# Optimization experiments

Hardware: AMD Instinct MI355X
Metric: run time of the kernel (lower is better)

## Reference

```python
import jax, jax.numpy as jnp
import numpy as np

N_ENTITIES = 100000
EMBED_DIM = 128
N_EDGES = 1600000
LEAKY_SLOPE = 0.01  # nn.LeakyReLU default


def setup_inputs() -> dict:
    key = jax.random.key(0)
    k1, k2, k3, k4, k5, k6, k7, k8 = jax.random.split(key, 8)
    entity_embs = jax.random.normal(k1, (N_ENTITIES, EMBED_DIM), dtype=jnp.float32)
    adj_rows = jax.random.randint(k2, (N_EDGES,), 0, N_ENTITIES, dtype=jnp.int32)
    adj_cols = jax.random.randint(k3, (N_EDGES,), 0, N_ENTITIES, dtype=jnp.int32)
    adj_vals = jax.random.uniform(k4, (N_EDGES,), dtype=jnp.float32)
    s = 1.0 / np.sqrt(EMBED_DIM)  # nn.Linear default init scale
    W_self = jax.random.uniform(k5, (EMBED_DIM, EMBED_DIM), jnp.float32, -s, s)
    b_self = jax.random.uniform(k6, (EMBED_DIM,), jnp.float32, -s, s)
    W_neigh = jax.random.uniform(k7, (EMBED_DIM, EMBED_DIM), jnp.float32, -s, s)
    b_neigh = jax.random.uniform(k8, (EMBED_DIM,), jnp.float32, -s, s)
    return {"entity_embs": entity_embs, "adj_rows": adj_rows, "adj_cols": adj_cols,
            "adj_vals": adj_vals, "W_self": W_self, "b_self": b_self,
            "W_neigh": W_neigh, "b_neigh": b_neigh}


def reference(entity_embs, adj_rows, adj_cols, adj_vals, W_self, b_self, W_neigh, b_neigh):
    # self path: Linear(input_dim, output_dim) -> x @ W.T + b
    self_emb = entity_embs @ W_self.T + b_self  # [N, D]
    # neighbor path: sparse adjacency SpMM (COO): out[r] += v * embs[c]
    contrib = adj_vals[:, None] * entity_embs[adj_cols]  # [E, D]
    neigh = jax.ops.segment_sum(contrib, adj_rows, num_segments=N_ENTITIES)  # [N, D]
    neigh_emb = neigh @ W_neigh.T + b_neigh
    out = jax.nn.leaky_relu(self_emb + neigh_emb, negative_slope=LEAKY_SLOPE)
    # dropout is identity in eval mode
    return out
```

## Files before the change

kernel.cpp:

```cpp
#include <hip/hip_runtime.h>

#define DIM 128
#define TILE_R 32
#define CAP 64
#define NREG 8
#define NCHUNK 256

typedef __attribute__((ext_vector_type(8))) short short8;
typedef __attribute__((ext_vector_type(4))) float floatx4;

static __device__ __forceinline__ short f2bf(float x) {
    unsigned u = __float_as_uint(x);
    u = (u + 0x7FFF + ((u >> 16) & 1)) >> 16;
    return (short)u;
}
static __device__ __forceinline__ float bflo(unsigned p) { return __uint_as_float(p << 16); }
static __device__ __forceinline__ float bfhi(unsigned p) { return __uint_as_float(p & 0xFFFF0000u); }

static __device__ __forceinline__ unsigned packcv(int c, float v) {
    int q = (int)(v * 32768.f + 0.5f);
    q = q > 32767 ? 32767 : q;
    return ((unsigned)c << 15) | (unsigned)q;
}

__global__ __launch_bounds__(256) void zero_kernel(float4* __restrict__ out, int n4) {
    int i = blockIdx.x * 256 + threadIdx.x;
    if (i < n4) out[i] = make_float4(0.f, 0.f, 0.f, 0.f);
}

__global__ __launch_bounds__(256) void zero_counts_kernel(int* __restrict__ cnt,
                                                          int* __restrict__ cursor, int n) {
    int i = blockIdx.x * 256 + threadIdx.x;
    if (i < n) cnt[i] = 0;
    if (i == 0) *cursor = 0;
}

__global__ __launch_bounds__(256) void prep_kernel(const float* __restrict__ Wself,
                                                   const float* __restrict__ Wneigh,
                                                   short* __restrict__ Wf,
                                                   int* __restrict__ next, int nRows) {
    int idx = blockIdx.x * 256 + threadIdx.x;
    if (idx < 4096) {
        int t = idx >> 8;
        int s = (idx >> 6) & 3;
        int lane = idx & 63;
        int n = (t & 7) * 16 + (lane & 15);
        int k0 = s * 32 + (lane >> 4) * 8;
        const float* row = (t < 8 ? Wself : Wneigh) + (size_t)n * DIM + k0;
        short8 v;
#pragma unroll
        for (int j = 0; j < 8; j++) v[j] = f2bf(row[j]);
        *(short8*)(Wf + (size_t)idx * 8) = v;
    }
    int r = idx - 4096;
    if (r >= 0 && r < nRows) next[r] = r * CAP;
}

__global__ __launch_bounds__(256) void pack_kernel(const int* __restrict__ cols,
                                                   const float* __restrict__ vals,
                                                   unsigned* __restrict__ pe, int nE) {
    int i4 = (blockIdx.x * 256 + threadIdx.x) * 4;
    if (i4 + 3 < nE) {
        int4 c = *(const int4*)(cols + i4);
        float4 v = *(const float4*)(vals + i4);
        uint4 o;
        o.x = packcv(c.x, v.x);
        o.y = packcv(c.y, v.y);
        o.z = packcv(c.z, v.z);
        o.w = packcv(c.w, v.w);
        *(uint4*)(pe + i4) = o;
    } else {
        for (int k = 0; k < 4 && i4 + k < nE; k++) pe[i4 + k] = packcv(cols[i4 + k], vals[i4 + k]);
    }
}

__global__ __launch_bounds__(256) void fill_xcd_pk_kernel(const int* __restrict__ rows,
                                                          const unsigned* __restrict__ pe,
                                                          int* __restrict__ next,
                                                          unsigned* __restrict__ pk,
                                                          int nE, int nRows) {
    int region = blockIdx.x & (NREG - 1);
    int chunk = blockIdx.x / NREG;
    int rowsPerReg = (nRows + NREG - 1) / NREG;
    int rowLo = region * rowsPerReg;
    int rowHi = min(rowLo + rowsPerReg, nRows);
    int per = (nE + NCHUNK - 1) / NCHUNK;
    per = (per + 7) & ~7;
    int s = chunk * per;
    int e = min(s + per, nE);

    for (int base = s + threadIdx.x * 8; base < e; base += 256 * 8) {
        int r8[8];
        unsigned p8[8];
        int cnt = 8;
        if (base + 7 < e) {
            int4 rv0 = *(const int4*)(rows + base);
            int4 rv1 = *(const int4*)(rows + base + 4);
            uint4 pv0 = *(const uint4*)(pe + base);
            uint4 pv1 = *(const uint4*)(pe + base + 4);
            r8[0] = rv0.x; r8[1] = rv0.y; r8[2] = rv0.z; r8[3] = rv0.w;
            r8[4] = rv1.x; r8[5] = rv1.y; r8[6] = rv1.z; r8[7] = rv1.w;
            p8[0] = pv0.x; p8[1] = pv0.y; p8[2] = pv0.z; p8[3] = pv0.w;
            p8[4] = pv1.x; p8[5] = pv1.y; p8[6] = pv1.z; p8[7] = pv1.w;
        } else {
            cnt = e - base;
            for (int k = 0; k < cnt; k++) {
                r8[k] = rows[base + k];
                p8[k] = pe[base + k];
            }
        }
#pragma unroll 8
        for (int k = 0; k < cnt; k++) {
            int rr = r8[k];
            if (rr >= rowLo && rr < rowHi) {
                int p = atomicAdd(&next[rr], 1);
                if (p < rr * CAP + CAP) pk[p] = p8[k];
            }
        }
    }
}

__global__ __launch_bounds__(256) void hist_kernel(const int* __restrict__ rows,
                                                   int* __restrict__ cnt, int nE) {
    int i4 = (blockIdx.x * 256 + threadIdx.x) * 4;
    if (i4 + 3 < nE) {
        int4 r = *(const int4*)(rows + i4);
        atomicAdd(&cnt[r.x], 1);
        atomicAdd(&cnt[r.y], 1);
        atomicAdd(&cnt[r.z], 1);
        atomicAdd(&cnt[r.w], 1);
    } else {
        for (int k = 0; k < 4 && i4 + k < nE; k++) atomicAdd(&cnt[rows[i4 + k]], 1);
    }
}

__global__ __launch_bounds__(256) void offsets_kernel(int* __restrict__ next,
                                                      int* __restrict__ start,
                                                      int* __restrict__ cursor, int n) {
    int i = blockIdx.x * 256 + threadIdx.x;
    int lane = threadIdx.x & 63;
    int c = (i < n) ? next[i] : 0;
    int s = c;
#pragma unroll
    for (int d = 1; d < 64; d <<= 1) {
        int t = __shfl_up(s, d);
        if (lane >= d) s += t;
    }
    int total = __shfl(s, 63);
    int base = 0;
    if (lane == 63) base = atomicAdd(cursor, total);
    base = __shfl(base, 63);
    int off = base + s - c;
    if (i < n) {
        start[i] = off;
        next[i] = off;
    }
}

__global__ __launch_bounds__(256) void fillB_kernel(const int* __restrict__ rows,
                                                    const int* __restrict__ cols,
                                                    const float* __restrict__ vals,
                                                    int* __restrict__ next,
                                                    int2* __restrict__ csr, int nE) {
    int i4 = (blockIdx.x * 256 + threadIdx.x) * 4;
    if (i4 + 3 < nE) {
        int4 r = *(const int4*)(rows + i4);
        int4 c = *(const int4*)(cols + i4);
        float4 v = *(const float4*)(vals + i4);
        int p0 = atomicAdd(&next[r.x], 1);
        int p1 = atomicAdd(&next[r.y], 1);
        int p2 = atomicAdd(&next[r.z], 1);
        int p3 = atomicAdd(&next[r.w], 1);
        csr[p0] = make_int2(c.x, __float_as_int(v.x));
        csr[p1] = make_int2(c.y, __float_as_int(v.y));
        csr[p2] = make_int2(c.z, __float_as_int(v.z));
        csr[p3] = make_int2(c.w, __float_as_int(v.w));
    } else {
        for (int k = 0; k < 4 && i4 + k < nE; k++) {
            int p = atomicAdd(&next[rows[i4 + k]], 1);
            csr[p] = make_int2(cols[i4 + k], __float_as_int(vals[i4 + k]));
        }
    }
}

__global__ __launch_bounds__(256) void wprep_kernel(const float* __restrict__ Wself,
                                                    const float* __restrict__ Wneigh,
                                                    short* __restrict__ Wf) {
    int idx = blockIdx.x * 256 + threadIdx.x;
    int t = idx >> 8;
    int s = (idx >> 6) & 3;
    int lane = idx & 63;
    int n = (t & 7) * 16 + (lane & 15);
    int k0 = s * 32 + (lane >> 4) * 8;
    const float* row = (t < 8 ? Wself : Wneigh) + (size_t)n * DIM + k0;
    short8 v;
#pragma unroll
    for (int j = 0; j < 8; j++) v[j] = f2bf(row[j]);
    *(short8*)(Wf + (size_t)idx * 8) = v;
}

__global__ __launch_bounds__(256) void gemm4_kernel(const float* __restrict__ embs,
                                                    const short* __restrict__ Wf,
                                                    unsigned short* __restrict__ Sb,
                                                    unsigned short* __restrict__ Yb,
                                                    int nRows) {
    int wave = threadIdx.x >> 6;
    int lane = threadIdx.x & 63;
    int quad = lane >> 4;
    int m0 = blockIdx.x * 256 + wave * 64;

    short8 a[4][4];
#pragma unroll
    for (int rt = 0; rt < 4; rt++) {
        int m = m0 + rt * 16 + (lane & 15);
        bool valid = m < nRows;
        const float* Arow = embs + (size_t)m * DIM;
#pragma unroll
        for (int s = 0; s < 4; s++) {
            float4 f0 = make_float4(0.f, 0.f, 0.f, 0.f), f1 = f0;
            if (valid) {
                f0 = *(const float4*)(Arow + s * 32 + quad * 8);
                f1 = *(const float4*)(Arow + s * 32 + quad * 8 + 4);
            }
            short8 av;
            av[0] = f2bf(f0.x); av[1] = f2bf(f0.y); av[2] = f2bf(f0.z); av[3] = f2bf(f0.w);
            av[4] = f2bf(f1.x); av[5] = f2bf(f1.y); av[6] = f2bf(f1.z); av[7] = f2bf(f1.w);
            a[rt][s] = av;
        }
    }

    const short8* WfV = (const short8*)Wf;
#pragma unroll
    for (int t = 0; t < 16; t++) {
        floatx4 acc0 = {0.f, 0.f, 0.f, 0.f};
        floatx4 acc1 = acc0, acc2 = acc0, acc3 = acc0;
#pragma unroll
        for (int s = 0; s < 4; s++) {
            short8 b = WfV[(t * 4 + s) * 64 + lane];
            acc0 = __builtin_amdgcn_mfma_f32_16x16x32_bf16(a[0][s], b, acc0, 0, 0, 0);
            acc1 = __builtin_amdgcn_mfma_f32_16x16x32_bf16(a[1][s], b, acc1, 0, 0, 0);
            acc2 = __builtin_amdgcn_mfma_f32_16x16x32_bf16(a[2][s], b, acc2, 0, 0, 0);
            acc3 = __builtin_amdgcn_mfma_f32_16x16x32_bf16(a[3][s], b, acc3, 0, 0, 0);
        }
        int col = t * 16 + (lane & 15);
        unsigned short* dst = (col < DIM) ? (Sb + col) : (Yb + (col - DIM));
#pragma unroll
        for (int reg = 0; reg < 4; reg++) {
            int g0 = m0 + quad * 4 + reg;
            int g1 = g0 + 16, g2 = g0 + 32, g3 = g0 + 48;
            if (g0 < nRows) dst[(size_t)g0 * DIM] = (unsigned short)f2bf(acc0[reg]);
            if (g1 < nRows) dst[(size_t)g1 * DIM] = (unsigned short)f2bf(acc1[reg]);
            if (g2 < nRows) dst[(size_t)g2 * DIM] = (unsigned short)f2bf(acc2[reg]);
            if (g3 < nRows) dst[(size_t)g3 * DIM] = (unsigned short)f2bf(acc3[reg]);
        }
    }
}

__global__ __launch_bounds__(256) void gatherY_pk_kernel(const unsigned* __restrict__ Sb,
                                                         const unsigned* __restrict__ Yb,
                                                         const int* __restrict__ rowEnd,
                                                         const unsigned* __restrict__ pk,
                                                         const float* __restrict__ bself,
                                                         const float* __restrict__ bneigh,
                                                         float* __restrict__ out, int nRows) {
    int r = blockIdx.x * 4 + (threadIdx.x >> 6);
    if (r >= nRows) return;
    int lane = threadIdx.x & 63;
    int s = r * CAP;
    int e = min(__builtin_amdgcn_readfirstlane(rowEnd[r]), s + CAP);
    float ax = 0.f, ay = 0.f;
    const float qs = 1.f / 32768.f;
    int j = s;
    for (; j + 4 <= e; j += 4) {
        uint4 q = *(const uint4*)(pk + j);
        unsigned y0 = Yb[(size_t)(q.x >> 15) * 64 + lane];
        unsigned y1 = Yb[(size_t)(q.y >> 15) * 64 + lane];
        unsigned y2 = Yb[(size_t)(q.z >> 15) * 64 + lane];
        unsigned y3 = Yb[(size_t)(q.w >> 15) * 64 + lane];
        float v0 = (float)(q.x & 32767u) * qs;
        float v1 = (float)(q.y & 32767u) * qs;
        float v2 = (float)(q.z & 32767u) * qs;
        float v3 = (float)(q.w & 32767u) * qs;
        ax += v0 * bflo(y0) + v1 * bflo(y1) + v2 * bflo(y2) + v3 * bflo(y3);
        ay += v0 * bfhi(y0) + v1 * bfhi(y1) + v2 * bfhi(y2) + v3 * bfhi(y3);
    }
    for (; j < e; j++) {
        unsigned q = pk[j];
        float v = (float)(q & 32767u) * qs;
        unsigned y = Yb[(size_t)(q >> 15) * 64 + lane];
        ax += v * bflo(y);
        ay += v * bfhi(y);
    }
    unsigned sp = __builtin_nontemporal_load(&Sb[(size_t)r * 64 + lane]);
    float ox = bflo(sp) + bself[2 * lane] + bneigh[2 * lane] + ax;
    float oy = bfhi(sp) + bself[2 * lane + 1] + bneigh[2 * lane + 1] + ay;
    ox = ox > 0.f ? ox : 0.01f * ox;
    oy = oy > 0.f ? oy : 0.01f * oy;
    union { float2 f; double d; } u;
    u.f = make_float2(ox, oy);
    __builtin_nontemporal_store(u.d, (double*)(out + (size_t)r * DIM + lane * 2));
}

__global__ __launch_bounds__(256) void gatherY_kernel(const unsigned* __restrict__ Sb,
                                                      const unsigned* __restrict__ Yb,
                                                      const int* __restrict__ start,
                                                      const int* __restrict__ next,
                                                      const int2* __restrict__ csr,
                                                      const float* __restrict__ bself,
                                                      const float* __restrict__ bneigh,
                                                      float* __restrict__ out, int nRows) {
    int r = blockIdx.x * 4 + (threadIdx.x >> 6);
    if (r >= nRows) return;
    int lane = threadIdx.x & 63;
    int s = __builtin_amdgcn_readfirstlane(start[r]);
    int e = __builtin_amdgcn_readfirstlane(next[r]);
    float ax = 0.f, ay = 0.f;
    int j = s;
    for (; j + 4 <= e; j += 4) {
        int2 c0 = csr[j], c1 = csr[j + 1], c2 = csr[j + 2], c3 = csr[j + 3];
        unsigned y0 = Yb[(size_t)c0.x * 64 + lane];
        unsigned y1 = Yb[(size_t)c1.x * 64 + lane];
        unsigned y2 = Yb[(size_t)c2.x * 64 + lane];
        unsigned y3 = Yb[(size_t)c3.x * 64 + lane];
        float v0 = __int_as_float(c0.y), v1 = __int_as_float(c1.y);
        float v2 = __int_as_float(c2.y), v3 = __int_as_float(c3.y);
        ax += v0 * bflo(y0) + v1 * bflo(y1) + v2 * bflo(y2) + v3 * bflo(y3);
        ay += v0 * bfhi(y0) + v1 * bfhi(y1) + v2 * bfhi(y2) + v3 * bfhi(y3);
    }
    for (; j < e; j++) {
        int2 c = csr[j];
        float v = __int_as_float(c.y);
        unsigned y = Yb[(size_t)c.x * 64 + lane];
        ax += v * bflo(y);
        ay += v * bfhi(y);
    }
    unsigned sp = __builtin_nontemporal_load(&Sb[(size_t)r * 64 + lane]);
    float ox = bflo(sp) + bself[2 * lane] + bneigh[2 * lane] + ax;
    float oy = bfhi(sp) + bself[2 * lane + 1] + bneigh[2 * lane + 1] + ay;
    ox = ox > 0.f ? ox : 0.01f * ox;
    oy = oy > 0.f ? oy : 0.01f * oy;
    union { float2 f; double d; } u;
    u.f = make_float2(ox, oy);
    __builtin_nontemporal_store(u.d, (double*)(out + (size_t)r * DIM + lane * 2));
}

__global__ __launch_bounds__(256) void gather_embs_kernel(const float2* __restrict__ embs2,
                                                          const int* __restrict__ start,
                                                          const int* __restrict__ next,
                                                          const int2* __restrict__ csr,
                                                          float* __restrict__ out, int nRows) {
    int r = blockIdx.x * 4 + (threadIdx.x >> 6);
    if (r >= nRows) return;
    int lane = threadIdx.x & 63;
    int s = start[r];
    int e = next[r];
    float2 acc = make_float2(0.f, 0.f);
    for (int b = s; b < e; b += 64) {
        int n = min(64, e - b);
        int2 cv = make_int2(0, 0);
        if (lane < n) cv = csr[b + lane];
        float vf = __int_as_float(cv.y);
        for (int j = 0; j < n; j++) {
            int cj = __shfl(cv.x, j);
            float vj = __shfl(vf, j);
            float2 x = embs2[(size_t)cj * 64 + lane];
            acc.x += vj * x.x;
            acc.y += vj * x.y;
        }
    }
    ((float2*)out)[(size_t)r * 64 + lane] = acc;
}

__global__ __launch_bounds__(256) void scatter_kernel(
    const float* __restrict__ embs, const int* __restrict__ rows,
    const int* __restrict__ cols, const float* __restrict__ vals,
    float* __restrict__ out, int nE) {
    int e = blockIdx.x * 4 + (threadIdx.x >> 6);
    if (e >= nE) return;
    int lane = threadIdx.x & 63;
    int r = rows[e];
    int c = cols[e];
    float v = vals[e];
    float2 x = ((const float2*)(embs + (size_t)c * DIM))[lane];
    float* dst = out + (size_t)r * DIM + lane * 2;
    unsafeAtomicAdd(dst, v * x.x);
    unsafeAtomicAdd(dst + 1, v * x.y);
}

__global__ __launch_bounds__(256) void fused_kernel(
    const float* __restrict__ embs, const float* __restrict__ Wself,
    const float* __restrict__ bself, const float* __restrict__ Wneigh,
    const float* __restrict__ bneigh, float* __restrict__ out, int nRows) {
    __shared__ float xs[TILE_R][DIM];
    __shared__ float xn[TILE_R][DIM];

    int r0 = blockIdx.x * TILE_R;
    if (r0 >= nRows) return;

    const float4* gs = (const float4*)(embs + (size_t)r0 * DIM);
    const float4* gn = (const float4*)(out + (size_t)r0 * DIM);
    float4* sxs = (float4*)&xs[0][0];
    float4* sxn = (float4*)&xn[0][0];
    for (int i = threadIdx.x; i < TILE_R * DIM / 4; i += 256) {
        sxs[i] = gs[i];
        sxn[i] = gn[i];
    }
    __syncthreads();

    int j = threadIdx.x & 127;
    int rbase = (threadIdx.x >> 7) * 16;

    const float4* ws = (const float4*)(Wself + (size_t)j * DIM);
    const float4* wn = (const float4*)(Wneigh + (size_t)j * DIM);

    float acc[16];
#pragma unroll
    for (int i = 0; i < 16; i++) acc[i] = 0.f;

    for (int k4 = 0; k4 < DIM / 4; k4++) {
        float4 a = ws[k4];
        float4 b = wn[k4];
#pragma unroll
        for (int rr = 0; rr < 16; rr++) {
            float4 x = *(const float4*)&xs[rbase + rr][k4 * 4];
            float4 y = *(const float4*)&xn[rbase + rr][k4 * 4];
            acc[rr] += x.x * a.x + x.y * a.y + x.z * a.z + x.w * a.w
                     + y.x * b.x + y.y * b.y + y.z * b.z + y.w * b.w;
        }
    }

    float bias = bself[j] + bneigh[j];
#pragma unroll
    for (int rr = 0; rr < 16; rr++) {
        float v = acc[rr] + bias;
        out[(size_t)(r0 + rbase + rr) * DIM + j] = v > 0.f ? v : 0.01f * v;
    }
}

static inline size_t a16(size_t x) { return (x + 15) & ~(size_t)15; }

extern "C" void kernel_launch(void* const* d_in, const int* in_sizes, int n_in,
                              void* d_out, int out_size, void* d_ws, size_t ws_size,
                              hipStream_t stream) {
    const float* embs   = (const float*)d_in[0];
    const int*   rows   = (const int*)d_in[1];
    const int*   cols   = (const int*)d_in[2];
    const float* vals   = (const float*)d_in[3];
    const float* Wself  = (const float*)d_in[4];
    const float* bself  = (const float*)d_in[5];
    const float* Wneigh = (const float*)d_in[6];
    const float* bneigh = (const float*)d_in[7];
    float* out = (float*)d_out;

    int nE = in_sizes[1];
    int nRows = out_size / DIM;
    size_t wfBytes = (size_t)16 * 4 * 64 * 8 * 2;
    size_t bfPlane = (size_t)nRows * DIM * 2;

    size_t A7_next = 0;
    size_t A7_buck = A7_next + a16((size_t)nRows * 4);
    size_t A7_pe   = A7_buck + a16((size_t)nRows * CAP * 4);
    size_t A7_wf   = A7_pe + a16((size_t)nE * 4);
    size_t A7_y    = A7_wf + a16(wfBytes);
    size_t A7_s    = A7_y + bfPlane;
    size_t needA7  = A7_s + bfPlane;
    bool   okA7    = nRows <= (1 << 17);

    size_t B_next  = 0;
    size_t B_start = B_next + a16((size_t)nRows * 4);
    size_t B_cur   = B_start + a16((size_t)nRows * 4);
    size_t B_csr   = B_cur + 16;
    size_t B_wf    = B_csr + a16((size_t)nE * 8);
    size_t B_y     = B_wf + a16(wfBytes);
    size_t B_s     = B_y + bfPlane;
    size_t needB   = B_s + bfPlane;

    size_t C_csr  = a16((size_t)(2 * nRows + 1) * 4);
    size_t needC  = C_csr + (size_t)nE * 8;

    int rb = (nRows + 255) / 256;
    int eb4 = (nE / 4 + 255) / 256;
    int ebp = ((nE + 3) / 4 + 255) / 256;

    if (okA7 && ws_size >= needA7) {
        int*      next = (int*)((char*)d_ws + A7_next);
        unsigned* pk   = (unsigned*)((char*)d_ws + A7_buck);
        unsigned* pe   = (unsigned*)((char*)d_ws + A7_pe);
        short*    Wf   = (short*)((char*)d_ws + A7_wf);
        unsigned short* Yb = (unsigned short*)((char*)d_ws + A7_y);
        unsigned short* Sb = (unsigned short*)((char*)d_ws + A7_s);

        prep_kernel<<<(4096 + nRows + 255) / 256, 256, 0, stream>>>(Wself, Wneigh, Wf, next, nRows);
        pack_kernel<<<ebp, 256, 0, stream>>>(cols, vals, pe, nE);
        fill_xcd_pk_kernel<<<NREG * NCHUNK, 256, 0, stream>>>(rows, pe, next, pk, nE, nRows);
        gemm4_kernel<<<(nRows + 255) / 256, 256, 0, stream>>>(embs, Wf, Sb, Yb, nRows);
        gatherY_pk_kernel<<<(nRows + 3) / 4, 256, 0, stream>>>(
            (const unsigned*)Sb, (const unsigned*)Yb, next, pk, bself, bneigh, out, nRows);
    } else if (ws_size >= needB) {
        int*  next   = (int*)((char*)d_ws + B_next);
        int*  start  = (int*)((char*)d_ws + B_start);
        int*  cursor = (int*)((char*)d_ws + B_cur);
        int2* csr    = (int2*)((char*)d_ws + B_csr);
        short* Wf    = (short*)((char*)d_ws + B_wf);
        unsigned short* Yb = (unsigned short*)((char*)d_ws + B_y);
        unsigned short* Sb = (unsigned short*)((char*)d_ws + B_s);

        zero_counts_kernel<<<rb, 256, 0, stream>>>(next, cursor, nRows);
        hist_kernel<<<eb4, 256, 0, stream>>>(rows, next, nE);
        offsets_kernel<<<rb, 256, 0, stream>>>(next, start, cursor, nRows);
        fillB_kernel<<<eb4, 256, 0, stream>>>(rows, cols, vals, next, csr, nE);
        wprep_kernel<<<16, 256, 0, stream>>>(Wself, Wneigh, Wf);
        gemm4_kernel<<<(nRows + 255) / 256, 256, 0, stream>>>(embs, Wf, Sb, Yb, nRows);
        gatherY_kernel<<<(nRows + 3) / 4, 256, 0, stream>>>(
            (const unsigned*)Sb, (const unsigned*)Yb, start, next, csr,
            bself, bneigh, out, nRows);
    } else if (ws_size >= needC) {
        int* next = (int*)d_ws;
        int* start = next + nRows;
        int* cursor = start + nRows;
        int2* csr = (int2*)((char*)d_ws + C_csr);

        zero_counts_kernel<<<rb, 256, 0, stream>>>(next, cursor, nRows);
        hist_kernel<<<eb4, 256, 0, stream>>>(rows, next, nE);
        offsets_kernel<<<rb, 256, 0, stream>>>(next, start, cursor, nRows);
        fillB_kernel<<<eb4, 256, 0, stream>>>(rows, cols, vals, next, csr, nE);
        gather_embs_kernel<<<(nRows + 3) / 4, 256, 0, stream>>>(
            (const float2*)embs, start, next, csr, out, nRows);
        fused_kernel<<<(nRows + TILE_R - 1) / TILE_R, 256, 0, stream>>>(
            embs, Wself, bself, Wneigh, bneigh, out, nRows);
    } else {
        int n4 = out_size / 4;
        zero_kernel<<<(n4 + 255) / 256, 256, 0, stream>>>((float4*)out, n4);
        scatter_kernel<<<(nE + 3) / 4, 256, 0, stream>>>(embs, rows, cols, vals, out, nE);
        fused_kernel<<<(nRows + TILE_R - 1) / TILE_R, 256, 0, stream>>>(
            embs, Wself, bself, Wneigh, bneigh, out, nRows);
    }
}
```

Measured before the change: 295.0 us.

## Merge pack/prep kernels and run fill alongside GEMM in one launch

Combines the weight-prep/next-init kernel with the edge packing kernel into one launch, and combines the bucket-fill atomics with the bf16 MFMA GEMM in a single kernel whose first blocks do the GEMM and the remaining blocks do the fill. This drops two launches and lets the compute-bound GEMM overlap with the atomic-bound fill. The cost is that the GEMM blocks occupy registers that may reduce fill occupancy, and the block ordering decides how much the two phases actually overlap.

```diff
diff --git a/kernel.cpp b/kernel.cpp
--- a/kernel.cpp
+++ b/kernel.cpp
@@ -35,10 +35,14 @@
     if (i == 0) *cursor = 0;
 }
 
-__global__ __launch_bounds__(256) void prep_kernel(const float* __restrict__ Wself,
-                                                   const float* __restrict__ Wneigh,
-                                                   short* __restrict__ Wf,
-                                                   int* __restrict__ next, int nRows) {
+__global__ __launch_bounds__(256) void packprep_kernel(const int* __restrict__ cols,
+                                                       const float* __restrict__ vals,
+                                                       unsigned* __restrict__ pe,
+                                                       const float* __restrict__ Wself,
+                                                       const float* __restrict__ Wneigh,
+                                                       short* __restrict__ Wf,
+                                                       int* __restrict__ next,
+                                                       int nE, int nRows) {
     int idx = blockIdx.x * 256 + threadIdx.x;
     if (idx < 4096) {
         int t = idx >> 8;
@@ -54,12 +58,8 @@
     }
     int r = idx - 4096;
     if (r >= 0 && r < nRows) next[r] = r * CAP;
-}
-
-__global__ __launch_bounds__(256) void pack_kernel(const int* __restrict__ cols,
-                                                   const float* __restrict__ vals,
-                                                   unsigned* __restrict__ pe, int nE) {
-    int i4 = (blockIdx.x * 256 + threadIdx.x) * 4;
+
+    int i4 = idx * 4;
     if (i4 + 3 < nE) {
         int4 c = *(const int4*)(cols + i4);
         float4 v = *(const float4*)(vals + i4);
@@ -74,47 +74,106 @@
     }
 }
 
-__global__ __launch_bounds__(256) void fill_xcd_pk_kernel(const int* __restrict__ rows,
-                                                          const unsigned* __restrict__ pe,
-                                                          int* __restrict__ next,
-                                                          unsigned* __restrict__ pk,
-                                                          int nE, int nRows) {
-    int region = blockIdx.x & (NREG - 1);
-    int chunk = blockIdx.x / NREG;
-    int rowsPerReg = (nRows + NREG - 1) / NREG;
-    int rowLo = region * rowsPerReg;
-    int rowHi = min(rowLo + rowsPerReg, nRows);
-    int per = (nE + NCHUNK - 1) / NCHUNK;
-    per = (per + 7) & ~7;
-    int s = chunk * per;
-    int e = min(s + per, nE);
-
-    for (int base = s + threadIdx.x * 8; base < e; base += 256 * 8) {
-        int r8[8];
-        unsigned p8[8];
-        int cnt = 8;
-        if (base + 7 < e) {
-            int4 rv0 = *(const int4*)(rows + base);
-            int4 rv1 = *(const int4*)(rows + base + 4);
-            uint4 pv0 = *(const uint4*)(pe + base);
-            uint4 pv1 = *(const uint4*)(pe + base + 4);
-            r8[0] = rv0.x; r8[1] = rv0.y; r8[2] = rv0.z; r8[3] = rv0.w;
-            r8[4] = rv1.x; r8[5] = rv1.y; r8[6] = rv1.z; r8[7] = rv1.w;
-            p8[0] = pv0.x; p8[1] = pv0.y; p8[2] = pv0.z; p8[3] = pv0.w;
-            p8[4] = pv1.x; p8[5] = pv1.y; p8[6] = pv1.z; p8[7] = pv1.w;
-        } else {
-            cnt = e - base;
+__global__ __launch_bounds__(256) void fillgemm_kernel(const int* __restrict__ rows,
+                                                       const unsigned* __restrict__ pe,
+                                                       int* __restrict__ next,
+                                                       unsigned* __restrict__ pk,
+                                                       int nE, int nRows,
+                                                       const float* __restrict__ embs,
+                                                       const short* __restrict__ Wf,
+                                                       unsigned short* __restrict__ Sb,
+                                                       unsigned short* __restrict__ Yb,
+                                                       int gemmBlocks) {
+    if ((int)blockIdx.x < gemmBlocks) {
+        int wave = threadIdx.x >> 6;
+        int lane = threadIdx.x & 63;
+        int quad = lane >> 4;
+        int m0 = blockIdx.x * 256 + wave * 64;
+
+        short8 a[4][4];
+#pragma unroll
+        for (int rt = 0; rt < 4; rt++) {
+            int m = m0 + rt * 16 + (lane & 15);
+            bool valid = m < nRows;
+            const float* Arow = embs + (size_t)m * DIM;
+#pragma unroll
+            for (int s = 0; s < 4; s++) {
+                float4 f0 = make_float4(0.f, 0.f, 0.f, 0.f), f1 = f0;
+                if (valid) {
+                    f0 = *(const float4*)(Arow + s * 32 + quad * 8);
+                    f1 = *(const float4*)(Arow + s * 32 + quad * 8 + 4);
+                }
+                short8 av;
+                av[0] = f2bf(f0.x); av[1] = f2bf(f0.y); av[2] = f2bf(f0.z); av[3] = f2bf(f0.w);
+                av[4] = f2bf(f1.x); av[5] = f2bf(f1.y); av[6] = f2bf(f1.z); av[7] = f2bf(f1.w);
+                a[rt][s] = av;
+            }
+        }
+
+        const short8* WfV = (const short8*)Wf;
+#pragma unroll
+        for (int t = 0; t < 16; t++) {
+            floatx4 acc0 = {0.f, 0.f, 0.f, 0.f};
+            floatx4 acc1 = acc0, acc2 = acc0, acc3 = acc0;
+#pragma unroll
+            for (int s = 0; s < 4; s++) {
+                short8 b = WfV[(t * 4 + s) * 64 + lane];
+                acc0 = __builtin_amdgcn_mfma_f32_16x16x32_bf16(a[0][s], b, acc0, 0, 0, 0);
+                acc1 = __builtin_amdgcn_mfma_f32_16x16x32_bf16(a[1][s], b, acc1, 0, 0, 0);
+                acc2 = __builtin_amdgcn_mfma_f32_16x16x32_bf16(a[2][s], b, acc2, 0, 0, 0);
+                acc3 = __builtin_amdgcn_mfma_f32_16x16x32_bf16(a[3][s], b, acc3, 0, 0, 0);
+            }
+            int col = t * 16 + (lane & 15);
+            unsigned short* dst = (col < DIM) ? (Sb + col) : (Yb + (col - DIM));
+#pragma unroll
+            for (int reg = 0; reg < 4; reg++) {
+                int g0 = m0 + quad * 4 + reg;
+                int g1 = g0 + 16, g2 = g0 + 32, g3 = g0 + 48;
+                if (g0 < nRows) dst[(size_t)g0 * DIM] = (unsigned short)f2bf(acc0[reg]);
+                if (g1 < nRows) dst[(size_t)g1 * DIM] = (unsigned short)f2bf(acc1[reg]);
+                if (g2 < nRows) dst[(size_t)g2 * DIM] = (unsigned short)f2bf(acc2[reg]);
+                if (g3 < nRows) dst[(size_t)g3 * DIM] = (unsigned short)f2bf(acc3[reg]);
+            }
+        }
+    } else {
+        int bid = blockIdx.x - gemmBlocks;
+        int region = bid & (NREG - 1);
+        int chunk = bid / NREG;
+        int rowsPerReg = (nRows + NREG - 1) / NREG;
+        int rowLo = region * rowsPerReg;
+        int rowHi = min(rowLo + rowsPerReg, nRows);
+        int per = (nE + NCHUNK - 1) / NCHUNK;
+        per = (per + 7) & ~7;
+        int s = chunk * per;
+        int e = min(s + per, nE);
+
+        for (int base = s + threadIdx.x * 8; base < e; base += 256 * 8) {
+            int r8[8];
+            unsigned p8[8];
+            int cnt = 8;
+            if (base + 7 < e) {
+                int4 rv0 = *(const int4*)(rows + base);
+                int4 rv1 = *(const int4*)(rows + base + 4);
+                uint4 pv0 = *(const uint4*)(pe + base);
+                uint4 pv1 = *(const uint4*)(pe + base + 4);
+                r8[0] = rv0.x; r8[1] = rv0.y; r8[2] = rv0.z; r8[3] = rv0.w;
+                r8[4] = rv1.x; r8[5] = rv1.y; r8[6] = rv1.z; r8[7] = rv1.w;
+                p8[0] = pv0.x; p8[1] = pv0.y; p8[2] = pv0.z; p8[3] = pv0.w;
+                p8[4] = pv1.x; p8[5] = pv1.y; p8[6] = pv1.z; p8[7] = pv1.w;
+            } else {
+                cnt = e - base;
+                for (int k = 0; k < cnt; k++) {
+                    r8[k] = rows[base + k];
+                    p8[k] = pe[base + k];
+                }
+            }
+#pragma unroll 8
             for (int k = 0; k < cnt; k++) {
-                r8[k] = rows[base + k];
-                p8[k] = pe[base + k];
-            }
-        }
-#pragma unroll 8
-        for (int k = 0; k < cnt; k++) {
-            int rr = r8[k];
-            if (rr >= rowLo && rr < rowHi) {
-                int p = atomicAdd(&next[rr], 1);
-                if (p < rr * CAP + CAP) pk[p] = p8[k];
+                int rr = r8[k];
+                if (rr >= rowLo && rr < rowHi) {
+                    int p = atomicAdd(&next[rr], 1);
+                    if (p < rr * CAP + CAP) pk[p] = p8[k];
+                }
             }
         }
     }
@@ -457,14 +516,14 @@
     size_t wfBytes = (size_t)16 * 4 * 64 * 8 * 2;
     size_t bfPlane = (size_t)nRows * DIM * 2;
 
-    size_t A7_next = 0;
-    size_t A7_buck = A7_next + a16((size_t)nRows * 4);
-    size_t A7_pe   = A7_buck + a16((size_t)nRows * CAP * 4);
-    size_t A7_wf   = A7_pe + a16((size_t)nE * 4);
-    size_t A7_y    = A7_wf + a16(wfBytes);
-    size_t A7_s    = A7_y + bfPlane;
-    size_t needA7  = A7_s + bfPlane;
-    bool   okA7    = nRows <= (1 << 17);
+    size_t A9_next = 0;
+    size_t A9_buck = A9_next + a16((size_t)nRows * 4);
+    size_t A9_pe   = A9_buck + a16((size_t)nRows * CAP * 4);
+    size_t A9_wf   = A9_pe + a16((size_t)nE * 4);
+    size_t A9_y    = A9_wf + a16(wfBytes);
+    size_t A9_s    = A9_y + bfPlane;
+    size_t needA9  = A9_s + bfPlane;
+    bool   okA9    = nRows <= (1 << 17);
 
     size_t B_next  = 0;
     size_t B_start = B_next + a16((size_t)nRows * 4);
@@ -482,18 +541,23 @@
     int eb4 = (nE / 4 + 255) / 256;
     int ebp = ((nE + 3) / 4 + 255) / 256;
 
-    if (okA7 && ws_size >= needA7) {
-        int*      next = (int*)((char*)d_ws + A7_next);
-        unsigned* pk   = (unsigned*)((char*)d_ws + A7_buck);
-        unsigned* pe   = (unsigned*)((char*)d_ws + A7_pe);
-        short*    Wf   = (short*)((char*)d_ws + A7_wf);
-        unsigned short* Yb = (unsigned short*)((char*)d_ws + A7_y);
-        unsigned short* Sb = (unsigned short*)((char*)d_ws + A7_s);
-
-        prep_kernel<<<(4096 + nRows + 255) / 256, 256, 0, stream>>>(Wself, Wneigh, Wf, next, nRows);
-        pack_kernel<<<ebp, 256, 0, stream>>>(cols, vals, pe, nE);
-        fill_xcd_pk_kernel<<<NREG * NCHUNK, 256, 0, stream>>>(rows, pe, next, pk, nE, nRows);
-        gemm4_kernel<<<(nRows + 255) / 256, 256, 0, stream>>>(embs, Wf, Sb, Yb, nRows);
+    if (okA9 && ws_size >= needA9) {
+        int*      next = (int*)((char*)d_ws + A9_next);
+        unsigned* pk   = (unsigned*)((char*)d_ws + A9_buck);
+        unsigned* pe   = (unsigned*)((char*)d_ws + A9_pe);
+        short*    Wf   = (short*)((char*)d_ws + A9_wf);
+        unsigned short* Yb = (unsigned short*)((char*)d_ws + A9_y);
+        unsigned short* Sb = (unsigned short*)((char*)d_ws + A9_s);
+
+        int ppBlocks = ebp;
+        int ppMin = (4096 + nRows + 255) / 256;
+        if (ppBlocks < ppMin) ppBlocks = ppMin;
+        int gemmBlocks = (nRows + 255) / 256;
+
+        packprep_kernel<<<ppBlocks, 256, 0, stream>>>(cols, vals, pe, Wself, Wneigh,
+                                                      Wf, next, nE, nRows);
+        fillgemm_kernel<<<gemmBlocks + NREG * NCHUNK, 256, 0, stream>>>(
+            rows, pe, next, pk, nE, nRows, embs, Wf, Sb, Yb, gemmBlocks);
         gatherY_pk_kernel<<<(nRows + 3) / 4, 256, 0, stream>>>(
             (const unsigned*)Sb, (const unsigned*)Yb, next, pk, bself, bneigh, out, nRows);
     } else if (ws_size >= needB) {
```

After: 306.0 us. 3.7% more time.
